# Kernel optimization log

Hardware: AMD Instinct MI355X
Metric: run time of the kernel (lower is better)

The kernel has to match this reference:

```python
import jax, jax.numpy as jnp
import numpy as np

N, A, C = 4096, 512, 100


def setup_inputs() -> dict:
    key = jax.random.key(0)
    k1, k2, k3 = jax.random.split(key, 3)
    features = jax.random.normal(k1, (N, A), dtype=jnp.float32)
    y_s = jax.random.normal(k2, (N, C), dtype=jnp.float32)
    labels = jax.random.randint(k3, (N,), 0, C, dtype=jnp.int64)
    CoVariance = jnp.zeros((C, A, A), dtype=jnp.float32)
    Ave = jnp.zeros((C, A), dtype=jnp.float32)
    Amount = jnp.zeros((C,), dtype=jnp.float32)
    return {"features": features, "y_s": y_s, "CoVariance": CoVariance,
            "Ave": Ave, "Amount": Amount, "labels": labels}


def reference(features, y_s, CoVariance, Ave, Amount, labels):
    n, a = features.shape
    c = Ave.shape[0]
    dt = features.dtype

    onehot = jax.nn.one_hot(labels, c, dtype=dt)            # [N, C]
    counts = onehot.sum(axis=0)                             # [C]
    counts_safe = jnp.where(counts == 0, 1.0, counts)       # Amount_CxA==0 -> 1

    # per-class mean: ave_CxA [C, A]
    sum_feats = onehot.T @ features                          # [C, A]
    ave_CxA = sum_feats / counts_safe[:, None]

    # centered features w.r.t. own-class mean; masked per-class copies
    centered = features - ave_CxA[labels]                    # [N, A]
    masked = onehot.T[:, :, None] * centered[None, :, :]     # [C, N, A]
    # per-class scatter of outer products (equals torch bmm over zero-padded rows)
    var_temp = jnp.einsum('cna,nb->cab', masked, centered) / counts_safe[:, None, None]

    # mixing weights; NaN (0/0) -> 0
    denom = counts + Amount                                  # [C]
    w = jnp.where(denom > 0, counts / denom, 0.0)            # [C]

    ave_old = jax.lax.stop_gradient(Ave)                     # .detach() in torch
    cov_old = jax.lax.stop_gradient(CoVariance)
    diff = ave_old - ave_CxA                                 # [C, A]
    additional_CV = (w * (1.0 - w))[:, None, None] * jnp.einsum('ca,cb->cab', diff, diff)

    new_cov = cov_old * (1.0 - w)[:, None, None] + var_temp * w[:, None, None] + additional_CV
    new_ave = ave_old * (1.0 - w)[:, None] + ave_CxA * w[:, None]
    new_amount = Amount + counts

    logp = jax.nn.log_softmax(y_s, axis=-1)                  # [N, C]
    loss = -jnp.mean(jnp.take_along_axis(logp, labels[:, None], axis=1))

    return loss, new_cov, new_ave, new_amount
```

## Files before the change

kernel.cpp:

```cpp
#include <hip/hip_runtime.h>


#define TM 128
#define KC 16
#define LSTR 132
#define LZ 8

typedef float nf4 __attribute__((ext_vector_type(4)));
typedef float f2  __attribute__((ext_vector_type(2)));

__global__ __launch_bounds__(256) void mega_kernel(
    const float* __restrict__ feats, const float* __restrict__ cov_in,
    const float* __restrict__ Ave_in, const float* __restrict__ y_s,
    const int* __restrict__ labels, const float* __restrict__ Amount,
    float* __restrict__ out_cov, float* __restrict__ out_ave,
    float* __restrict__ out_amt, float* __restrict__ out_loss0,
    int N, int C, int A, float invN, int AZ) {

    const int nxy = gridDim.x * gridDim.y;
    const int bxy = blockIdx.y * gridDim.x + blockIdx.x;
    const int tid = threadIdx.x;

    if ((int)blockIdx.z < LZ) {
        __shared__ float bsum[4];
        const int lane = tid & 63;
        const int wv = tid >> 6;
        const int bid = (int)blockIdx.z * nxy + bxy;
        const int nwaves = LZ * nxy * 4;
        const int gw = bid * 4 + wv;
        float wsum = 0.f;
        for (int r = gw; r < N; r += nwaves) {
            const float* row = y_s + (size_t)r * C;
            float m = -1e30f;
            for (int col = lane; col < C; col += 64) m = fmaxf(m, row[col]);
            #pragma unroll
            for (int off = 32; off > 0; off >>= 1) m = fmaxf(m, __shfl_xor(m, off));
            float se = 0.f;
            for (int col = lane; col < C; col += 64) se += __expf(row[col] - m);
            #pragma unroll
            for (int off = 32; off > 0; off >>= 1) se += __shfl_xor(se, off);
            if (lane == 0) wsum += -(row[labels[r]] - m - __logf(se));
        }
        if (lane == 0) bsum[wv] = wsum;
        __syncthreads();
        if (tid == 0)
            atomicAdd(out_loss0, (bsum[0] + bsum[1] + bsum[2] + bsum[3]) * invN);
        return;
    }

    if ((int)blockIdx.z < LZ + AZ) {
        __shared__ int idxs[256];
        __shared__ int acnt;
        const int bid = ((int)blockIdx.z - LZ) * nxy + bxy;
        if (bid >= C) return;
        const int c = bid;
        if (tid == 0) acnt = 0;
        __syncthreads();
        for (int i = tid; i < N; i += 256)
            if (labels[i] == c) { int p = atomicAdd(&acnt, 1); if (p < 256) idxs[p] = i; }
        __syncthreads();
        const int nc = min(acnt, 256);
        const float cf = (float)nc;
        const float ic = 1.f / fmaxf(cf, 1.f);
        const float am = Amount[c];
        const float dn = cf + am;
        const float w = dn > 0.f ? cf / dn : 0.f;
        if (tid == 0) out_amt[c] = am + cf;
        for (int c0 = 0; c0 < A; c0 += 512) {
            const int colA = c0 + tid;
            const int colB = c0 + 256 + tid;
            float s0 = 0.f, s1 = 0.f;
            int j = 0;
            for (; j + 3 < nc; j += 4) {
                const float* f0 = feats + (size_t)idxs[j] * A;
                const float* f1 = feats + (size_t)idxs[j + 1] * A;
                const float* f2p = feats + (size_t)idxs[j + 2] * A;
                const float* f3 = feats + (size_t)idxs[j + 3] * A;
                if (colA < A) s0 += f0[colA] + f1[colA] + f2p[colA] + f3[colA];
                if (colB < A) s1 += f0[colB] + f1[colB] + f2p[colB] + f3[colB];
            }
            for (; j < nc; ++j) {
                const float* fr = feats + (size_t)idxs[j] * A;
                if (colA < A) s0 += fr[colA];
                if (colB < A) s1 += fr[colB];
            }
            if (colA < A)
                out_ave[(size_t)c * A + colA] =
                    Ave_in[(size_t)c * A + colA] * (1.f - w) + (s0 * ic) * w;
            if (colB < A)
                out_ave[(size_t)c * A + colB] =
                    Ave_in[(size_t)c * A + colB] * (1.f - w) + (s1 * ic) * w;
        }
        return;
    }

    const int c  = (int)blockIdx.z - LZ - AZ;
    const int a0 = blockIdx.y * TM;
    const int b0 = blockIdx.x * TM;

    __shared__ float Xs[2][2][KC][LSTR];
    __shared__ float muA[TM], muB[TM], dA[TM], dB[TM];
    __shared__ int idxbuf[256];
    __shared__ int ccnt;

    const int ty = tid >> 4, tx = tid & 15;
    const int ty4 = ty * 4, tx4 = tx * 4;

    if (tid == 0) ccnt = 0;
    __syncthreads();
    for (int i = tid; i < N; i += 256)
        if (labels[i] == c) { int p = atomicAdd(&ccnt, 1); if (p < 256) idxbuf[p] = i; }
    __syncthreads();
    const int nc = min(ccnt, 256);

    const float cf  = (float)nc;
    const float ic  = 1.f / fmaxf(cf, 1.f);
    const float am  = Amount[c];
    const float dn  = cf + am;
    const float w   = dn > 0.f ? cf / dn : 0.f;
    const float omw = 1.f - w;
    const float s   = ic * w;
    const float aw  = w * omw;
    const size_t cbase = (size_t)c * A * A;

    if (s > 0.f) {
        const int nchunks = (nc + KC - 1) / KC;
        const int li = ty;
        const int cg = tx4;

        float4 v0, v1, v2, v3;
        auto LOADV = [&](int ch) {
            const int slot = ch * KC + li;
            v0 = make_float4(0.f, 0.f, 0.f, 0.f); v1 = v0; v2 = v0; v3 = v0;
            if (slot < nc) {
                int row = idxbuf[slot];
                const float* fr = feats + (size_t)row * A;
                v0 = *reinterpret_cast<const float4*>(fr + a0 + cg);
                v1 = *reinterpret_cast<const float4*>(fr + a0 + cg + 64);
                v2 = *reinterpret_cast<const float4*>(fr + b0 + cg);
                v3 = *reinterpret_cast<const float4*>(fr + b0 + cg + 64);
            }
        };
        auto STORE_LDS = [&](int b) {
            *reinterpret_cast<float4*>(&Xs[b][0][li][cg])      = v0;
            *reinterpret_cast<float4*>(&Xs[b][0][li][cg + 64]) = v1;
            *reinterpret_cast<float4*>(&Xs[b][1][li][cg])      = v2;
            *reinterpret_cast<float4*>(&Xs[b][1][li][cg + 64]) = v3;
        };

        f2 acc[2][4][2][2] = {};
        if (omw != 0.f) {
            const float sc = omw / s;
            #pragma unroll
            for (int ri = 0; ri < 2; ++ri)
                #pragma unroll
                for (int i = 0; i < 4; ++i) {
                    const size_t rowo = cbase + (size_t)(a0 + ri * 64 + ty4 + i) * A + b0;
                    #pragma unroll
                    for (int ci = 0; ci < 2; ++ci) {
                        float4 co = *reinterpret_cast<const float4*>(&cov_in[rowo + ci * 64 + tx4]);
                        f2 t0; t0.x = co.x * sc; t0.y = co.y * sc;
                        f2 t1; t1.x = co.z * sc; t1.y = co.w * sc;
                        acc[ri][i][ci][0] = t0;
                        acc[ri][i][ci][1] = t1;
                    }
                }
        }

        float csum = 0.f;
        const int cside = tid >> 7;
        const int ccol  = tid & 127;

        LOADV(0);
        STORE_LDS(0);

        for (int ch = 0; ch < nchunks; ++ch) {
            const int cur = ch & 1;
            __syncthreads();
            if (ch + 1 < nchunks) LOADV(ch + 1);

            const int kn = min(KC, nc - ch * KC);
            if (kn == KC) {
                #pragma unroll
                for (int k = 0; k < KC; ++k) {
                    float4 a0v = *reinterpret_cast<const float4*>(&Xs[cur][0][k][ty4]);
                    float4 a1v = *reinterpret_cast<const float4*>(&Xs[cur][0][k][64 + ty4]);
                    float4 b0v = *reinterpret_cast<const float4*>(&Xs[cur][1][k][tx4]);
                    float4 b1v = *reinterpret_cast<const float4*>(&Xs[cur][1][k][64 + tx4]);
                    float af[2][4] = {{a0v.x, a0v.y, a0v.z, a0v.w}, {a1v.x, a1v.y, a1v.z, a1v.w}};
                    f2 bf[2][2];
                    bf[0][0].x = b0v.x; bf[0][0].y = b0v.y;
                    bf[0][1].x = b0v.z; bf[0][1].y = b0v.w;
                    bf[1][0].x = b1v.x; bf[1][0].y = b1v.y;
                    bf[1][1].x = b1v.z; bf[1][1].y = b1v.w;
                    #pragma unroll
                    for (int ri = 0; ri < 2; ++ri)
                        #pragma unroll
                        for (int i = 0; i < 4; ++i) {
                            f2 av; av.x = af[ri][i]; av.y = af[ri][i];
                            #pragma unroll
                            for (int ci = 0; ci < 2; ++ci) {
                                acc[ri][i][ci][0] = __builtin_elementwise_fma(av, bf[ci][0], acc[ri][i][ci][0]);
                                acc[ri][i][ci][1] = __builtin_elementwise_fma(av, bf[ci][1], acc[ri][i][ci][1]);
                            }
                        }
                }
            } else {
                for (int k = 0; k < kn; ++k) {
                    float4 a0v = *reinterpret_cast<const float4*>(&Xs[cur][0][k][ty4]);
                    float4 a1v = *reinterpret_cast<const float4*>(&Xs[cur][0][k][64 + ty4]);
                    float4 b0v = *reinterpret_cast<const float4*>(&Xs[cur][1][k][tx4]);
                    float4 b1v = *reinterpret_cast<const float4*>(&Xs[cur][1][k][64 + tx4]);
                    float af[2][4] = {{a0v.x, a0v.y, a0v.z, a0v.w}, {a1v.x, a1v.y, a1v.z, a1v.w}};
                    f2 bf[2][2];
                    bf[0][0].x = b0v.x; bf[0][0].y = b0v.y;
                    bf[0][1].x = b0v.z; bf[0][1].y = b0v.w;
                    bf[1][0].x = b1v.x; bf[1][0].y = b1v.y;
                    bf[1][1].x = b1v.z; bf[1][1].y = b1v.w;
                    #pragma unroll
                    for (int ri = 0; ri < 2; ++ri)
                        #pragma unroll
                        for (int i = 0; i < 4; ++i) {
                            f2 av; av.x = af[ri][i]; av.y = af[ri][i];
                            #pragma unroll
                            for (int ci = 0; ci < 2; ++ci) {
                                acc[ri][i][ci][0] = __builtin_elementwise_fma(av, bf[ci][0], acc[ri][i][ci][0]);
                                acc[ri][i][ci][1] = __builtin_elementwise_fma(av, bf[ci][1], acc[ri][i][ci][1]);
                            }
                        }
                }
            }

            for (int k = 0; k < kn; ++k) csum += Xs[cur][cside][k][ccol];

            if (ch + 1 < nchunks) STORE_LDS(cur ^ 1);
        }

        {
            float mu = csum * ic;
            if (tid < 128) {
                muA[ccol] = mu;
                dA[ccol] = Ave_in[(size_t)c * A + a0 + ccol] - mu;
            } else {
                muB[ccol] = mu;
                dB[ccol] = Ave_in[(size_t)c * A + b0 + ccol] - mu;
            }
        }
        __syncthreads();

        float mb[2][4], db[2][4];
        #pragma unroll
        for (int ci = 0; ci < 2; ++ci)
            #pragma unroll
            for (int j = 0; j < 4; ++j) {
                mb[ci][j] = muB[ci * 64 + tx4 + j];
                db[ci][j] = dB[ci * 64 + tx4 + j];
            }

        #pragma unroll
        for (int ri = 0; ri < 2; ++ri)
            #pragma unroll
            for (int i = 0; i < 4; ++i) {
                float ma = w  * muA[ri * 64 + ty4 + i];
                float da = aw * dA[ri * 64 + ty4 + i];
                const size_t rowo = cbase + (size_t)(a0 + ri * 64 + ty4 + i) * A + b0;
                #pragma unroll
                for (int ci = 0; ci < 2; ++ci) {
                    nf4 res;
                    res.x = acc[ri][i][ci][0].x * s - ma * mb[ci][0] + da * db[ci][0];
                    res.y = acc[ri][i][ci][0].y * s - ma * mb[ci][1] + da * db[ci][1];
                    res.z = acc[ri][i][ci][1].x * s - ma * mb[ci][2] + da * db[ci][2];
                    res.w = acc[ri][i][ci][1].y * s - ma * mb[ci][3] + da * db[ci][3];
                    __builtin_nontemporal_store(res,
                        reinterpret_cast<nf4*>(&out_cov[rowo + ci * 64 + tx4]));
                }
            }
    } else {
        for (int t = tid; t < TM * TM / 4; t += 256) {
            const int r = t >> 5;
            const int c4 = (t & 31) * 4;
            const size_t o = cbase + (size_t)(a0 + r) * A + b0 + c4;
            float4 co = *reinterpret_cast<const float4*>(&cov_in[o]);
            nf4 res;
            res.x = co.x * omw; res.y = co.y * omw; res.z = co.z * omw; res.w = co.w * omw;
            __builtin_nontemporal_store(res, reinterpret_cast<nf4*>(&out_cov[o]));
        }
    }
}

extern "C" void kernel_launch(void* const* d_in, const int* in_sizes, int n_in,
                              void* d_out, int out_size, void* d_ws, size_t ws_size,
                              hipStream_t stream) {
    const float* feats  = (const float*)d_in[0];
    const float* y_s    = (const float*)d_in[1];
    const float* cov_in = (const float*)d_in[2];
    const float* Ave_in = (const float*)d_in[3];
    const float* Amount = (const float*)d_in[4];
    const int*   labels = (const int*)d_in[5];

    const int C = in_sizes[4];
    const int N = in_sizes[5];
    const int A = in_sizes[3] / C;

    float* out      = (float*)d_out;
    float* out_loss = out;
    float* out_cov  = out + 1;
    float* out_ave  = out_cov + (size_t)C * A * A;
    float* out_amt  = out_ave + (size_t)C * A;

    hipMemsetAsync(out_loss, 0, sizeof(float), stream);

    const int nxy = (A / TM) * (A / TM);
    const int AZ = (C + nxy - 1) / nxy;
    dim3 grid(A / TM, A / TM, LZ + AZ + C);
    mega_kernel<<<grid, 256, 0, stream>>>(feats, cov_in, Ave_in, y_s, labels, Amount,
                                          out_cov, out_ave, out_amt, out_loss,
                                          N, C, A, 1.f / (float)N, AZ);
}
```

Measured before the change: 218.1 us.

## Exploit covariance symmetry by computing only upper-triangle tiles and mirroring

The per-class covariance tiles are now enumerated only for upper-triangle tile pairs, and each off-diagonal block writes its transposed result through an LDS staging buffer. Diagonal tiles load features once and reuse them for both operands. The old-covariance blend moves from accumulator initialisation to the store epilogue. This reduces outer-product FMA work and feature loads, at the cost of extra LDS transposes, syncs, and fewer but heavier blocks.

```diff
diff --git a/kernel.cpp b/kernel.cpp
--- a/kernel.cpp
+++ b/kernel.cpp
@@ -95,8 +95,12 @@
     }
 
     const int c  = (int)blockIdx.z - LZ - AZ;
-    const int a0 = blockIdx.y * TM;
-    const int b0 = blockIdx.x * TM;
+    int ai = 0, rem = (int)blockIdx.x, span = A / TM;
+    while (rem >= span) { rem -= span; ++ai; --span; }
+    const int bi = ai + rem;
+    const bool diag = (ai == bi);
+    const int a0 = ai * TM;
+    const int b0 = bi * TM;
 
     __shared__ float Xs[2][2][KC][LSTR];
     __shared__ float muA[TM], muB[TM], dA[TM], dB[TM];
@@ -137,38 +141,25 @@
                 const float* fr = feats + (size_t)row * A;
                 v0 = *reinterpret_cast<const float4*>(fr + a0 + cg);
                 v1 = *reinterpret_cast<const float4*>(fr + a0 + cg + 64);
-                v2 = *reinterpret_cast<const float4*>(fr + b0 + cg);
-                v3 = *reinterpret_cast<const float4*>(fr + b0 + cg + 64);
+                if (!diag) {
+                    v2 = *reinterpret_cast<const float4*>(fr + b0 + cg);
+                    v3 = *reinterpret_cast<const float4*>(fr + b0 + cg + 64);
+                }
             }
         };
         auto STORE_LDS = [&](int b) {
             *reinterpret_cast<float4*>(&Xs[b][0][li][cg])      = v0;
             *reinterpret_cast<float4*>(&Xs[b][0][li][cg + 64]) = v1;
-            *reinterpret_cast<float4*>(&Xs[b][1][li][cg])      = v2;
-            *reinterpret_cast<float4*>(&Xs[b][1][li][cg + 64]) = v3;
+            if (!diag) {
+                *reinterpret_cast<float4*>(&Xs[b][1][li][cg])      = v2;
+                *reinterpret_cast<float4*>(&Xs[b][1][li][cg + 64]) = v3;
+            }
         };
 
         f2 acc[2][4][2][2] = {};
-        if (omw != 0.f) {
-            const float sc = omw / s;
-            #pragma unroll
-            for (int ri = 0; ri < 2; ++ri)
-                #pragma unroll
-                for (int i = 0; i < 4; ++i) {
-                    const size_t rowo = cbase + (size_t)(a0 + ri * 64 + ty4 + i) * A + b0;
-                    #pragma unroll
-                    for (int ci = 0; ci < 2; ++ci) {
-                        float4 co = *reinterpret_cast<const float4*>(&cov_in[rowo + ci * 64 + tx4]);
-                        f2 t0; t0.x = co.x * sc; t0.y = co.y * sc;
-                        f2 t1; t1.x = co.z * sc; t1.y = co.w * sc;
-                        acc[ri][i][ci][0] = t0;
-                        acc[ri][i][ci][1] = t1;
-                    }
-                }
-        }
 
         float csum = 0.f;
-        const int cside = tid >> 7;
+        const int side = diag ? 0 : (tid >> 7);
         const int ccol  = tid & 127;
 
         LOADV(0);
@@ -179,59 +170,34 @@
             __syncthreads();
             if (ch + 1 < nchunks) LOADV(ch + 1);
 
+            const float (*XA)[LSTR] = Xs[cur][0];
+            const float (*XB)[LSTR] = diag ? Xs[cur][0] : Xs[cur][1];
             const int kn = min(KC, nc - ch * KC);
-            if (kn == KC) {
+            for (int k = 0; k < kn; ++k) {
+                float4 a0v = *reinterpret_cast<const float4*>(&XA[k][ty4]);
+                float4 a1v = *reinterpret_cast<const float4*>(&XA[k][64 + ty4]);
+                float4 b0v = *reinterpret_cast<const float4*>(&XB[k][tx4]);
+                float4 b1v = *reinterpret_cast<const float4*>(&XB[k][64 + tx4]);
+                float af[2][4] = {{a0v.x, a0v.y, a0v.z, a0v.w}, {a1v.x, a1v.y, a1v.z, a1v.w}};
+                f2 bf[2][2];
+                bf[0][0].x = b0v.x; bf[0][0].y = b0v.y;
+                bf[0][1].x = b0v.z; bf[0][1].y = b0v.w;
+                bf[1][0].x = b1v.x; bf[1][0].y = b1v.y;
+                bf[1][1].x = b1v.z; bf[1][1].y = b1v.w;
                 #pragma unroll
-                for (int k = 0; k < KC; ++k) {
-                    float4 a0v = *reinterpret_cast<const float4*>(&Xs[cur][0][k][ty4]);
-                    float4 a1v = *reinterpret_cast<const float4*>(&Xs[cur][0][k][64 + ty4]);
-                    float4 b0v = *reinterpret_cast<const float4*>(&Xs[cur][1][k][tx4]);
-                    float4 b1v = *reinterpret_cast<const float4*>(&Xs[cur][1][k][64 + tx4]);
-                    float af[2][4] = {{a0v.x, a0v.y, a0v.z, a0v.w}, {a1v.x, a1v.y, a1v.z, a1v.w}};
-                    f2 bf[2][2];
-                    bf[0][0].x = b0v.x; bf[0][0].y = b0v.y;
-                    bf[0][1].x = b0v.z; bf[0][1].y = b0v.w;
-                    bf[1][0].x = b1v.x; bf[1][0].y = b1v.y;
-                    bf[1][1].x = b1v.z; bf[1][1].y = b1v.w;
+                for (int ri = 0; ri < 2; ++ri)
                     #pragma unroll
-                    for (int ri = 0; ri < 2; ++ri)
+                    for (int i = 0; i < 4; ++i) {
+                        f2 av; av.x = af[ri][i]; av.y = af[ri][i];
                         #pragma unroll
-                        for (int i = 0; i < 4; ++i) {
-                            f2 av; av.x = af[ri][i]; av.y = af[ri][i];
-                            #pragma unroll
-                            for (int ci = 0; ci < 2; ++ci) {
-                                acc[ri][i][ci][0] = __builtin_elementwise_fma(av, bf[ci][0], acc[ri][i][ci][0]);
-                                acc[ri][i][ci][1] = __builtin_elementwise_fma(av, bf[ci][1], acc[ri][i][ci][1]);
-                            }
+                        for (int ci = 0; ci < 2; ++ci) {
+                            acc[ri][i][ci][0] = __builtin_elementwise_fma(av, bf[ci][0], acc[ri][i][ci][0]);
+                            acc[ri][i][ci][1] = __builtin_elementwise_fma(av, bf[ci][1], acc[ri][i][ci][1]);
                         }
-                }
-            } else {
-                for (int k = 0; k < kn; ++k) {
-                    float4 a0v = *reinterpret_cast<const float4*>(&Xs[cur][0][k][ty4]);
-                    float4 a1v = *reinterpret_cast<const float4*>(&Xs[cur][0][k][64 + ty4]);
-                    float4 b0v = *reinterpret_cast<const float4*>(&Xs[cur][1][k][tx4]);
-                    float4 b1v = *reinterpret_cast<const float4*>(&Xs[cur][1][k][64 + tx4]);
-                    float af[2][4] = {{a0v.x, a0v.y, a0v.z, a0v.w}, {a1v.x, a1v.y, a1v.z, a1v.w}};
-                    f2 bf[2][2];
-                    bf[0][0].x = b0v.x; bf[0][0].y = b0v.y;
-                    bf[0][1].x = b0v.z; bf[0][1].y = b0v.w;
-                    bf[1][0].x = b1v.x; bf[1][0].y = b1v.y;
-                    bf[1][1].x = b1v.z; bf[1][1].y = b1v.w;
-                    #pragma unroll
-                    for (int ri = 0; ri < 2; ++ri)
-                        #pragma unroll
-                        for (int i = 0; i < 4; ++i) {
-                            f2 av; av.x = af[ri][i]; av.y = af[ri][i];
-                            #pragma unroll
-                            for (int ci = 0; ci < 2; ++ci) {
-                                acc[ri][i][ci][0] = __builtin_elementwise_fma(av, bf[ci][0], acc[ri][i][ci][0]);
-                                acc[ri][i][ci][1] = __builtin_elementwise_fma(av, bf[ci][1], acc[ri][i][ci][1]);
-                            }
-                        }
-                }
-            }
-
-            for (int k = 0; k < kn; ++k) csum += Xs[cur][cside][k][ccol];
+                    }
+            }
+
+            for (int k = 0; k < kn; ++k) csum += Xs[cur][side][k][ccol];
 
             if (ch + 1 < nchunks) STORE_LDS(cur ^ 1);
         }
@@ -263,27 +229,90 @@
             for (int i = 0; i < 4; ++i) {
                 float ma = w  * muA[ri * 64 + ty4 + i];
                 float da = aw * dA[ri * 64 + ty4 + i];
+                #pragma unroll
+                for (int ci = 0; ci < 2; ++ci) {
+                    acc[ri][i][ci][0].x = acc[ri][i][ci][0].x * s - ma * mb[ci][0] + da * db[ci][0];
+                    acc[ri][i][ci][0].y = acc[ri][i][ci][0].y * s - ma * mb[ci][1] + da * db[ci][1];
+                    acc[ri][i][ci][1].x = acc[ri][i][ci][1].x * s - ma * mb[ci][2] + da * db[ci][2];
+                    acc[ri][i][ci][1].y = acc[ri][i][ci][1].y * s - ma * mb[ci][3] + da * db[ci][3];
+                }
+            }
+
+        #pragma unroll
+        for (int ri = 0; ri < 2; ++ri)
+            #pragma unroll
+            for (int i = 0; i < 4; ++i) {
                 const size_t rowo = cbase + (size_t)(a0 + ri * 64 + ty4 + i) * A + b0;
                 #pragma unroll
                 for (int ci = 0; ci < 2; ++ci) {
                     nf4 res;
-                    res.x = acc[ri][i][ci][0].x * s - ma * mb[ci][0] + da * db[ci][0];
-                    res.y = acc[ri][i][ci][0].y * s - ma * mb[ci][1] + da * db[ci][1];
-                    res.z = acc[ri][i][ci][1].x * s - ma * mb[ci][2] + da * db[ci][2];
-                    res.w = acc[ri][i][ci][1].y * s - ma * mb[ci][3] + da * db[ci][3];
+                    res.x = acc[ri][i][ci][0].x;
+                    res.y = acc[ri][i][ci][0].y;
+                    res.z = acc[ri][i][ci][1].x;
+                    res.w = acc[ri][i][ci][1].y;
+                    if (omw != 0.f) {
+                        float4 co = *reinterpret_cast<const float4*>(&cov_in[rowo + ci * 64 + tx4]);
+                        res.x += co.x * omw; res.y += co.y * omw;
+                        res.z += co.z * omw; res.w += co.w * omw;
+                    }
                     __builtin_nontemporal_store(res,
                         reinterpret_cast<nf4*>(&out_cov[rowo + ci * 64 + tx4]));
                 }
             }
+
+        if (!diag) {
+            float* tb = &Xs[0][0][0][0];
+            #pragma unroll
+            for (int cid = 0; cid < 4; ++cid) {
+                __syncthreads();
+                if ((ty >> 3) == (cid & 1)) {
+                    const int rb = (ty & 7) * 4;
+                    #pragma unroll
+                    for (int i = 0; i < 4; ++i)
+                        #pragma unroll
+                        for (int ci = 0; ci < 2; ++ci) {
+                            float* t0 = &tb[(rb + i) * LSTR + ci * 64 + tx4];
+                            t0[0] = acc[cid >> 1][i][ci][0].x;
+                            t0[1] = acc[cid >> 1][i][ci][0].y;
+                            t0[2] = acc[cid >> 1][i][ci][1].x;
+                            t0[3] = acc[cid >> 1][i][ci][1].y;
+                        }
+                }
+                __syncthreads();
+                const int bc = tid >> 1;
+                const int ar0 = (tid & 1) << 4;
+                const size_t orow = cbase + (size_t)(b0 + bc) * A + a0 + (cid << 5) + ar0;
+                #pragma unroll
+                for (int q = 0; q < 4; ++q) {
+                    nf4 res;
+                    res.x = tb[(ar0 + q * 4 + 0) * LSTR + bc];
+                    res.y = tb[(ar0 + q * 4 + 1) * LSTR + bc];
+                    res.z = tb[(ar0 + q * 4 + 2) * LSTR + bc];
+                    res.w = tb[(ar0 + q * 4 + 3) * LSTR + bc];
+                    if (omw != 0.f) {
+                        float4 co = *reinterpret_cast<const float4*>(&cov_in[orow + q * 4]);
+                        res.x += co.x * omw; res.y += co.y * omw;
+                        res.z += co.z * omw; res.w += co.w * omw;
+                    }
+                    __builtin_nontemporal_store(res,
+                        reinterpret_cast<nf4*>(&out_cov[orow + q * 4]));
+                }
+            }
+        }
     } else {
-        for (int t = tid; t < TM * TM / 4; t += 256) {
-            const int r = t >> 5;
-            const int c4 = (t & 31) * 4;
-            const size_t o = cbase + (size_t)(a0 + r) * A + b0 + c4;
-            float4 co = *reinterpret_cast<const float4*>(&cov_in[o]);
-            nf4 res;
-            res.x = co.x * omw; res.y = co.y * omw; res.z = co.z * omw; res.w = co.w * omw;
-            __builtin_nontemporal_store(res, reinterpret_cast<nf4*>(&out_cov[o]));
+        const int npass = diag ? 1 : 2;
+        for (int p = 0; p < npass; ++p) {
+            const int ra = p ? b0 : a0;
+            const int cb = p ? a0 : b0;
+            for (int t = tid; t < TM * TM / 4; t += 256) {
+                const int r = t >> 5;
+                const int c4 = (t & 31) * 4;
+                const size_t o = cbase + (size_t)(ra + r) * A + cb + c4;
+                float4 co = *reinterpret_cast<const float4*>(&cov_in[o]);
+                nf4 res;
+                res.x = co.x * omw; res.y = co.y * omw; res.z = co.z * omw; res.w = co.w * omw;
+                __builtin_nontemporal_store(res, reinterpret_cast<nf4*>(&out_cov[o]));
+            }
         }
     }
 }
@@ -310,9 +339,10 @@
 
     hipMemsetAsync(out_loss, 0, sizeof(float), stream);
 
-    const int nxy = (A / TM) * (A / TM);
-    const int AZ = (C + nxy - 1) / nxy;
-    dim3 grid(A / TM, A / TM, LZ + AZ + C);
+    const int nt = A / TM;
+    const int npairs = nt * (nt + 1) / 2;
+    const int AZ = (C + npairs - 1) / npairs;
+    dim3 grid(npairs, 1, LZ + AZ + C);
     mega_kernel<<<grid, 256, 0, stream>>>(feats, cov_in, Ave_in, y_s, labels, Amount,
                                           out_cov, out_ave, out_amt, out_loss,
                                           N, C, A, 1.f / (float)N, AZ);
```

After: 284.7 us. 1.31x slower.

## Exploit covariance symmetry: compute upper-triangle tiles and write transposed mirror

Applied to the files above, without the earlier changes.

Each class's covariance tile grid is reduced to the upper-triangular tile pairs. Off-diagonal tiles are transposed through shared memory and written to the mirrored location, which halves the outer-product accumulation work and the label scans. The old-covariance blend moves out of the accumulator initialisation into the epilogue. The cost is extra LDS staging, extra syncs and a non-temporal-free transposed store path. The grid also shrinks, so the AZ computation for the auxiliary blocks changes with it.

```diff
diff --git a/kernel.cpp b/kernel.cpp
--- a/kernel.cpp
+++ b/kernel.cpp
@@ -95,8 +95,12 @@
     }
 
     const int c  = (int)blockIdx.z - LZ - AZ;
-    const int a0 = blockIdx.y * TM;
-    const int b0 = blockIdx.x * TM;
+    int ai = 0, rem = (int)blockIdx.x, span = A / TM;
+    while (rem >= span) { rem -= span; ++ai; --span; }
+    const int bi = ai + rem;
+    const bool diag = (ai == bi);
+    const int a0 = ai * TM;
+    const int b0 = bi * TM;
 
     __shared__ float Xs[2][2][KC][LSTR];
     __shared__ float muA[TM], muB[TM], dA[TM], dB[TM];
@@ -149,23 +153,6 @@
         };
 
         f2 acc[2][4][2][2] = {};
-        if (omw != 0.f) {
-            const float sc = omw / s;
-            #pragma unroll
-            for (int ri = 0; ri < 2; ++ri)
-                #pragma unroll
-                for (int i = 0; i < 4; ++i) {
-                    const size_t rowo = cbase + (size_t)(a0 + ri * 64 + ty4 + i) * A + b0;
-                    #pragma unroll
-                    for (int ci = 0; ci < 2; ++ci) {
-                        float4 co = *reinterpret_cast<const float4*>(&cov_in[rowo + ci * 64 + tx4]);
-                        f2 t0; t0.x = co.x * sc; t0.y = co.y * sc;
-                        f2 t1; t1.x = co.z * sc; t1.y = co.w * sc;
-                        acc[ri][i][ci][0] = t0;
-                        acc[ri][i][ci][1] = t1;
-                    }
-                }
-        }
 
         float csum = 0.f;
         const int cside = tid >> 7;
@@ -257,33 +244,98 @@
                 db[ci][j] = dB[ci * 64 + tx4 + j];
             }
 
-        #pragma unroll
-        for (int ri = 0; ri < 2; ++ri)
-            #pragma unroll
-            for (int i = 0; i < 4; ++i) {
-                float ma = w  * muA[ri * 64 + ty4 + i];
-                float da = aw * dA[ri * 64 + ty4 + i];
-                const size_t rowo = cbase + (size_t)(a0 + ri * 64 + ty4 + i) * A + b0;
+        if (diag) {
+            #pragma unroll
+            for (int ri = 0; ri < 2; ++ri)
                 #pragma unroll
-                for (int ci = 0; ci < 2; ++ci) {
-                    nf4 res;
-                    res.x = acc[ri][i][ci][0].x * s - ma * mb[ci][0] + da * db[ci][0];
-                    res.y = acc[ri][i][ci][0].y * s - ma * mb[ci][1] + da * db[ci][1];
-                    res.z = acc[ri][i][ci][1].x * s - ma * mb[ci][2] + da * db[ci][2];
-                    res.w = acc[ri][i][ci][1].y * s - ma * mb[ci][3] + da * db[ci][3];
-                    __builtin_nontemporal_store(res,
-                        reinterpret_cast<nf4*>(&out_cov[rowo + ci * 64 + tx4]));
-                }
-            }
+                for (int i = 0; i < 4; ++i) {
+                    float ma = w  * muA[ri * 64 + ty4 + i];
+                    float da = aw * dA[ri * 64 + ty4 + i];
+                    const size_t rowo = cbase + (size_t)(a0 + ri * 64 + ty4 + i) * A + b0;
+                    #pragma unroll
+                    for (int ci = 0; ci < 2; ++ci) {
+                        nf4 res;
+                        res.x = acc[ri][i][ci][0].x * s - ma * mb[ci][0] + da * db[ci][0];
+                        res.y = acc[ri][i][ci][0].y * s - ma * mb[ci][1] + da * db[ci][1];
+                        res.z = acc[ri][i][ci][1].x * s - ma * mb[ci][2] + da * db[ci][2];
+                        res.w = acc[ri][i][ci][1].y * s - ma * mb[ci][3] + da * db[ci][3];
+                        if (omw != 0.f) {
+                            float4 co = *reinterpret_cast<const float4*>(&cov_in[rowo + ci * 64 + tx4]);
+                            res.x += co.x * omw; res.y += co.y * omw;
+                            res.z += co.z * omw; res.w += co.w * omw;
+                        }
+                        __builtin_nontemporal_store(res,
+                            reinterpret_cast<nf4*>(&out_cov[rowo + ci * 64 + tx4]));
+                    }
+                }
+        } else {
+            float* tb = &Xs[0][0][0][0];
+            #pragma unroll
+            for (int cid = 0; cid < 4; ++cid) {
+                const int ri = cid >> 1;
+                if ((ty >> 3) == (cid & 1)) {
+                    #pragma unroll
+                    for (int i = 0; i < 4; ++i) {
+                        const int lr = (ty & 7) * 4 + i;
+                        float ma = w  * muA[ri * 64 + ty4 + i];
+                        float da = aw * dA[ri * 64 + ty4 + i];
+                        const size_t rowo = cbase + (size_t)(a0 + cid * 32 + lr) * A + b0;
+                        #pragma unroll
+                        for (int ci = 0; ci < 2; ++ci) {
+                            float S0 = acc[ri][i][ci][0].x * s - ma * mb[ci][0] + da * db[ci][0];
+                            float S1 = acc[ri][i][ci][0].y * s - ma * mb[ci][1] + da * db[ci][1];
+                            float S2 = acc[ri][i][ci][1].x * s - ma * mb[ci][2] + da * db[ci][2];
+                            float S3 = acc[ri][i][ci][1].y * s - ma * mb[ci][3] + da * db[ci][3];
+                            float* t0 = &tb[lr * LSTR + ci * 64 + tx4];
+                            t0[0] = S0; t0[1] = S1; t0[2] = S2; t0[3] = S3;
+                            nf4 res; res.x = S0; res.y = S1; res.z = S2; res.w = S3;
+                            if (omw != 0.f) {
+                                float4 co = *reinterpret_cast<const float4*>(&cov_in[rowo + ci * 64 + tx4]);
+                                res.x += co.x * omw; res.y += co.y * omw;
+                                res.z += co.z * omw; res.w += co.w * omw;
+                            }
+                            __builtin_nontemporal_store(res,
+                                reinterpret_cast<nf4*>(&out_cov[rowo + ci * 64 + tx4]));
+                        }
+                    }
+                }
+                __syncthreads();
+                {
+                    const int bc = tid >> 1;
+                    const int ar0 = (tid & 1) << 4;
+                    const size_t orow = cbase + (size_t)(b0 + bc) * A + a0 + cid * 32 + ar0;
+                    #pragma unroll
+                    for (int q = 0; q < 4; ++q) {
+                        float4 res;
+                        res.x = tb[(ar0 + q * 4 + 0) * LSTR + bc];
+                        res.y = tb[(ar0 + q * 4 + 1) * LSTR + bc];
+                        res.z = tb[(ar0 + q * 4 + 2) * LSTR + bc];
+                        res.w = tb[(ar0 + q * 4 + 3) * LSTR + bc];
+                        if (omw != 0.f) {
+                            float4 co = *reinterpret_cast<const float4*>(&cov_in[orow + q * 4]);
+                            res.x += co.x * omw; res.y += co.y * omw;
+                            res.z += co.z * omw; res.w += co.w * omw;
+                        }
+                        *reinterpret_cast<float4*>(&out_cov[orow + q * 4]) = res;
+                    }
+                }
+                __syncthreads();
+            }
+        }
     } else {
-        for (int t = tid; t < TM * TM / 4; t += 256) {
-            const int r = t >> 5;
-            const int c4 = (t & 31) * 4;
-            const size_t o = cbase + (size_t)(a0 + r) * A + b0 + c4;
-            float4 co = *reinterpret_cast<const float4*>(&cov_in[o]);
-            nf4 res;
-            res.x = co.x * omw; res.y = co.y * omw; res.z = co.z * omw; res.w = co.w * omw;
-            __builtin_nontemporal_store(res, reinterpret_cast<nf4*>(&out_cov[o]));
+        const int npass = diag ? 1 : 2;
+        for (int p = 0; p < npass; ++p) {
+            const int ra = p ? b0 : a0;
+            const int cb = p ? a0 : b0;
+            for (int t = tid; t < TM * TM / 4; t += 256) {
+                const int r = t >> 5;
+                const int c4 = (t & 31) * 4;
+                const size_t o = cbase + (size_t)(ra + r) * A + cb + c4;
+                float4 co = *reinterpret_cast<const float4*>(&cov_in[o]);
+                nf4 res;
+                res.x = co.x * omw; res.y = co.y * omw; res.z = co.z * omw; res.w = co.w * omw;
+                __builtin_nontemporal_store(res, reinterpret_cast<nf4*>(&out_cov[o]));
+            }
         }
     }
 }
@@ -310,9 +362,10 @@
 
     hipMemsetAsync(out_loss, 0, sizeof(float), stream);
 
-    const int nxy = (A / TM) * (A / TM);
-    const int AZ = (C + nxy - 1) / nxy;
-    dim3 grid(A / TM, A / TM, LZ + AZ + C);
+    const int nt = A / TM;
+    const int npairs = nt * (nt + 1) / 2;
+    const int AZ = (C + npairs - 1) / npairs;
+    dim3 grid(npairs, 1, LZ + AZ + C);
     mega_kernel<<<grid, 256, 0, stream>>>(feats, cov_in, Ave_in, y_s, labels, Amount,
                                           out_cov, out_ave, out_amt, out_loss,
                                           N, C, A, 1.f / (float)N, AZ);
```

Measured after the change: 228.8 us. +4.9%, slower.
